# Kernel tuning notes

Measured on AMD Instinct MI355X. Metric: run time of the kernel, lower is better.

Reference implementation:

```python
import jax, jax.numpy as jnp
from jax import lax
import numpy as np

P = 0.25  # dropouto


def _lstm(x, Wih, Whh, b):
    """Standard torch-layout LSTM over [B, T, I]; gate order i,f,g,o.
    Wih: [4H, I], Whh: [4H, H], b: [4H] (= b_ih + b_hh). Returns [B, T, H]."""
    B, T, I = x.shape
    H = Whh.shape[1]
    # Precompute input contributions for all timesteps in one GEMM.
    xg = jnp.einsum('bti,gi->btg', x, Wih) + b  # [B, T, 4H]
    xg = jnp.swapaxes(xg, 0, 1)  # [T, B, 4H]

    def step(carry, xt):
        h, c = carry
        g = xt + h @ Whh.T  # [B, 4H]
        i, f, gg, o = jnp.split(g, 4, axis=-1)
        i = jax.nn.sigmoid(i)
        f = jax.nn.sigmoid(f)
        gg = jnp.tanh(gg)
        o = jax.nn.sigmoid(o)
        c = f * c + i * gg
        h = o * jnp.tanh(c)
        return (h, c), h

    h0 = jnp.zeros((B, H), x.dtype)
    c0 = jnp.zeros((B, H), x.dtype)
    _, hs = lax.scan(step, (h0, c0), xg)  # hs: [T, B, H]
    return jnp.swapaxes(hs, 0, 1)


def setup_inputs() -> dict:
    key = jax.random.key(0)
    ks = jax.random.split(key, 10)
    B, T = 512, 4096
    H1, H2 = 16, 1
    s = 0.25  # small init scale
    x = jax.random.normal(ks[0], (B, T, 1), jnp.float32)
    Wih1 = jax.random.normal(ks[1], (4 * H1, 1), jnp.float32) * s
    Whh1 = jax.random.normal(ks[2], (4 * H1, H1), jnp.float32) * s
    b1 = jax.random.normal(ks[3], (4 * H1,), jnp.float32) * s
    Wih2 = jax.random.normal(ks[4], (4 * H2, H1), jnp.float32) * s
    Whh2 = jax.random.normal(ks[5], (4 * H2, H2), jnp.float32) * s
    b2 = jax.random.normal(ks[6], (4 * H2,), jnp.float32) * s
    keep = 1.0 - P
    # Variational dropout masks: one mask per sequence, shared over time.
    mask1 = jax.random.bernoulli(ks[7], keep, (B, 1, H1)).astype(jnp.float32) / keep
    mask2 = jax.random.bernoulli(ks[8], keep, (B, 1, H2)).astype(jnp.float32) / keep
    return {"x": x, "Wih1": Wih1, "Whh1": Whh1, "b1": b1,
            "Wih2": Wih2, "Whh2": Whh2, "b2": b2,
            "mask1": mask1, "mask2": mask2}


def reference(x, Wih1, Whh1, b1, Wih2, Whh2, b2, mask1, mask2):
    out = _lstm(x, Wih1, Whh1, b1) * mask1   # dropouto on lstm1 output
    out = _lstm(out, Wih2, Whh2, b2) * mask2  # dropouto on lstm2 output
    return out  # [B, T, 1]
```

## Files before the change

### kernel.cpp

```cpp
#include <hip/hip_runtime.h>

typedef __fp16 f16x2 __attribute__((ext_vector_type(2)));

static __device__ __forceinline__ float rdlane(float v, int l) {
  return __uint_as_float(__builtin_amdgcn_readlane(__float_as_uint(v), (unsigned)l));
}
static __device__ __forceinline__ unsigned rdlane_u(unsigned v, int l) {
  return __builtin_amdgcn_readlane(v, (unsigned)l);
}

template <int CTRL>
static __device__ __forceinline__ float qperm(float v) {
  return __uint_as_float(__builtin_amdgcn_update_dpp(
      0u, __float_as_uint(v), CTRL, 0xF, 0xF, true));
}

static __device__ __forceinline__ float xswapadd32(float v) {
  float a = v, b;
  asm("v_mov_b32 %0, %1\n\t"
      "s_nop 1\n\t"
      "v_permlane32_swap_b32 %1, %0"
      : "=&v"(b), "+v"(a));
  return a + b;
}

static __device__ __forceinline__ float exp2a(float x) {
  float r;
  asm("v_exp_f32 %0, %1" : "=v"(r) : "v"(x));
  return r;
}
static __device__ __forceinline__ float rcpa(float x) {
  return __builtin_amdgcn_rcpf(x);
}

static __device__ __forceinline__ float dot2f(f16x2 a, unsigned bu, float c) {
#if __has_builtin(__builtin_amdgcn_fdot2)
  return __builtin_amdgcn_fdot2(a, __builtin_bit_cast(f16x2, bu), c, false);
#else
  float r = c;
  f16x2 b = __builtin_bit_cast(f16x2, bu);
  asm("v_dot2_f32_f16 %0, %1, %2, %0" : "+v"(r) : "v"(a), "v"(b));
  return r;
#endif
}

#define QP_XOR1 0xB1
#define QP_XOR2 0x4E
#define QP_XOR3 0x1B
#define QP_BC0  0x00
#define QP_BC1  0x55
#define QP_BC2  0xAA
#define QP_BC3  0xFF

__global__ __launch_bounds__(64, 1) void vdd_lstm_kernel(
    const float* __restrict__ x,
    const float* __restrict__ Wih1,
    const float* __restrict__ Whh1,
    const float* __restrict__ b1,
    const float* __restrict__ Wih2,
    const float* __restrict__ Whh2,
    const float* __restrict__ b2,
    const float* __restrict__ mask1,
    const float* __restrict__ mask2,
    float* __restrict__ out,
    int T) {
  const int b = blockIdx.x;
  const int lane = threadIdx.x;
  const int j = lane >> 2;
  const int gt = lane & 3;
  const int row = gt * 16 + j;

  const float LOG2E = 1.4426950408889634f;
  const bool isg = (gt == 2);
  const float sc = isg ? (-2.f * LOG2E) : (-LOG2E);
  const float aA = isg ? (-4.f * LOG2E) : 1.f;
  const float aC = isg ? (2.f * LOG2E) : 0.f;
  const bool isl1 = (lane == 1);

  f16x2 wh1[8];
#pragma unroll
  for (int m = 0; m < 8; ++m) {
    wh1[m].x = (__fp16)(Whh1[row * 16 + m] * sc);
    wh1[m].y = (__fp16)(Whh1[row * 16 + m + 8] * sc);
  }
  f16x2 wh2[8];
#pragma unroll
  for (int m = 0; m < 8; ++m) {
    wh2[m].x = (__fp16)(Wih2[gt * 16 + m] * mask1[b * 16 + m] * sc);
    wh2[m].y = (__fp16)(Wih2[gt * 16 + m + 8] * mask1[b * 16 + m + 8] * sc);
  }
  const float wih1 = Wih1[row] * sc;
  const float bb1  = b1[row] * sc;
  const float whh2 = Whh2[gt] * sc;
  const float bb2  = b2[gt] * sc;
  const float m2   = mask2[b];

  const float* xb = x + (size_t)b * T;
  float* ob = out + (size_t)b * T;

  float h = 0.f, cs = 0.f;
  float cs2 = 0.f, h2b = 0.f;

  const int NCH = T >> 6;
  const int tmax = T - 1;

  int idx0 = 1 + lane; idx0 = idx0 > tmax ? tmax : idx0;
  float xr = xb[idx0];

  {
    float x0 = xb[0];
    float pre = __fmaf_rn(wih1, x0, bb1);
    float a1 = __fmaf_rn(aA, rcpa(1.f + exp2a(pre)), aC);
    float g1 = qperm<QP_XOR2>(a1);
    float o1 = qperm<QP_XOR3>(a1);
    cs = a1 * g1;
    float th = __fmaf_rn(2.f, rcpa(1.f + exp2a(cs)), -1.f);
    h = o1 * th;
  }

  for (int ch = 0; ch < NCH; ++ch) {
    int idxn = (ch + 1) * 64 + 1 + lane;
    idxn = idxn > tmax ? tmax : idxn;
    float xnext = xb[idxn];

    float och = 0.f;

#pragma unroll 8
    for (int s = 0; s < 64; ++s) {
      float hsum = xswapadd32(h);
      float partner = hsum - h;
      f16x2 tp = __builtin_bit_cast(
          f16x2, __builtin_amdgcn_cvt_pkrtz(h, partner));
      unsigned tpu = __builtin_bit_cast(unsigned, tp);
      unsigned sp[8];
#pragma unroll
      for (int m = 0; m < 8; ++m) sp[m] = rdlane_u(tpu, 4 * m);

      float sx = rdlane(xr, s);

      float accA = __fmaf_rn(wih1, sx, bb1);
      float accB = dot2f(wh1[1], sp[1], 0.f);
      accA = dot2f(wh1[0], sp[0], accA);
      accB = dot2f(wh1[3], sp[3], accB);
      accA = dot2f(wh1[2], sp[2], accA);
      accB = dot2f(wh1[5], sp[5], accB);
      accA = dot2f(wh1[4], sp[4], accA);
      accB = dot2f(wh1[7], sp[7], accB);
      accA = dot2f(wh1[6], sp[6], accA);
      float pre = accA + accB;

      float accC = __fmaf_rn(whh2, h2b, bb2);
      float accD = dot2f(wh2[1], sp[1], 0.f);
      accC = dot2f(wh2[0], sp[0], accC);
      accD = dot2f(wh2[3], sp[3], accD);
      accC = dot2f(wh2[2], sp[2], accC);
      accD = dot2f(wh2[5], sp[5], accD);
      accC = dot2f(wh2[4], sp[4], accC);
      accD = dot2f(wh2[7], sp[7], accD);
      accC = dot2f(wh2[6], sp[6], accC);
      float pre2 = accC + accD;

      float a1 = __fmaf_rn(aA, rcpa(1.f + exp2a(pre)), aC);
      float f1 = qperm<QP_XOR1>(a1);
      float g1 = qperm<QP_XOR2>(a1);
      float o1 = qperm<QP_XOR3>(a1);
      cs = __fmaf_rn(f1, cs, a1 * g1);

      float a2 = __fmaf_rn(aA, rcpa(1.f + exp2a(pre2)), aC);
      float i2 = qperm<QP_BC0>(a2);
      float f2 = qperm<QP_BC1>(a2);
      float g2 = qperm<QP_BC2>(a2);
      float o2 = qperm<QP_BC3>(a2);
      cs2 = __fmaf_rn(f2, cs2, i2 * g2);

      float z = isl1 ? cs2 : cs;
      float thv = __fmaf_rn(2.f, rcpa(1.f + exp2a(z)), -1.f);
      float th2 = rdlane(thv, 1);
      float hn = o1 * thv;
      h2b = o2 * th2;
      float ov = h2b * m2;

      och = (lane == s) ? ov : och;
      h = hn;
    }

    ob[(ch << 6) + lane] = och;
    xr = xnext;
  }
}

extern "C" void kernel_launch(void* const* d_in, const int* in_sizes, int n_in,
                              void* d_out, int out_size, void* d_ws, size_t ws_size,
                              hipStream_t stream) {
  const float* x     = (const float*)d_in[0];
  const float* Wih1  = (const float*)d_in[1];
  const float* Whh1  = (const float*)d_in[2];
  const float* b1    = (const float*)d_in[3];
  const float* Wih2  = (const float*)d_in[4];
  const float* Whh2  = (const float*)d_in[5];
  const float* b2    = (const float*)d_in[6];
  const float* mask1 = (const float*)d_in[7];
  const float* mask2 = (const float*)d_in[8];
  float* out = (float*)d_out;

  const int B = in_sizes[8];
  const int T = in_sizes[0] / B;

  vdd_lstm_kernel<<<dim3(B), dim3(64), 0, stream>>>(
      x, Wih1, Whh1, b1, Wih2, Whh2, b2, mask1, mask2, out, T);
}
```

Baseline: 620.5 us.

## Skew LSTM2 one step behind LSTM1 to share a single tanh

Restructures the recurrence so layer 2 runs one timestep behind layer 1. Layer 2's pre-activation now takes the tanh of its cell state computed in the same lane-selected exp/rcp as layer 1's cell tanh, and its input dot products reuse the broadcast h vector. This moves layer 2's recurrent dependency off the serial critical path of each step. It adds a prologue step and shifted x indexing, and the output write alignment across chunk boundaries must stay correct.

```diff
diff --git a/kernel.cpp b/kernel.cpp
--- a/kernel.cpp
+++ b/kernel.cpp
@@ -98,18 +98,16 @@
   const float* xb = x + (size_t)b * T;
   float* ob = out + (size_t)b * T;
 
-  float h = 0.f, cs = 0.f;
-  float cs2 = 0.f, h2b = 0.f;
+  float h, cs;
+  float cs2p = 0.f;
+  float o2p = 0.f;
+  float och = 0.f;
 
   const int NCH = T >> 6;
   const int tmax = T - 1;
 
-  int idx0 = 1 + lane; idx0 = idx0 > tmax ? tmax : idx0;
-  float xr = xb[idx0];
-
   {
-    float x0 = xb[0];
-    float pre = __fmaf_rn(wih1, x0, bb1);
+    float pre = __fmaf_rn(wih1, xb[0], bb1);
     float a1 = __fmaf_rn(aA, rcpa(1.f + exp2a(pre)), aC);
     float g1 = qperm<QP_XOR2>(a1);
     float o1 = qperm<QP_XOR3>(a1);
@@ -118,74 +116,82 @@
     h = o1 * th;
   }
 
+  auto body = [&](float sx, bool doSel, int slot) {
+    float hsum = xswapadd32(h);
+    float partner = hsum - h;
+    f16x2 tp = __builtin_bit_cast(
+        f16x2, __builtin_amdgcn_cvt_pkrtz(h, partner));
+    unsigned tpu = __builtin_bit_cast(unsigned, tp);
+    unsigned sp[8];
+#pragma unroll
+    for (int m = 0; m < 8; ++m) sp[m] = rdlane_u(tpu, 4 * m);
+
+    float accA = __fmaf_rn(wih1, sx, bb1);
+    float accB = dot2f(wh1[1], sp[1], 0.f);
+    accA = dot2f(wh1[0], sp[0], accA);
+    accB = dot2f(wh1[3], sp[3], accB);
+    accA = dot2f(wh1[2], sp[2], accA);
+    accB = dot2f(wh1[5], sp[5], accB);
+    accA = dot2f(wh1[4], sp[4], accA);
+    accB = dot2f(wh1[7], sp[7], accB);
+    accA = dot2f(wh1[6], sp[6], accA);
+    float pre = accA + accB;
+
+    float accC = dot2f(wh2[0], sp[0], bb2);
+    float accD = dot2f(wh2[1], sp[1], 0.f);
+    accC = dot2f(wh2[2], sp[2], accC);
+    accD = dot2f(wh2[3], sp[3], accD);
+    accC = dot2f(wh2[4], sp[4], accC);
+    accD = dot2f(wh2[5], sp[5], accD);
+    accC = dot2f(wh2[6], sp[6], accC);
+    accD = dot2f(wh2[7], sp[7], accD);
+    float d2 = accC + accD;
+
+    float a1 = __fmaf_rn(aA, rcpa(1.f + exp2a(pre)), aC);
+    float f1 = qperm<QP_XOR1>(a1);
+    float g1 = qperm<QP_XOR2>(a1);
+    float o1 = qperm<QP_XOR3>(a1);
+    cs = __fmaf_rn(f1, cs, a1 * g1);
+
+    float z = isl1 ? cs2p : cs;
+    float thv = __fmaf_rn(2.f, rcpa(1.f + exp2a(z)), -1.f);
+    float hn = o1 * thv;
+    float th2 = rdlane(thv, 1);
+    float h2b = o2p * th2;
+
+    float pre2 = __fmaf_rn(whh2, h2b, d2);
+    float a2 = __fmaf_rn(aA, rcpa(1.f + exp2a(pre2)), aC);
+    float i2 = qperm<QP_BC0>(a2);
+    float f2 = qperm<QP_BC1>(a2);
+    float g2 = qperm<QP_BC2>(a2);
+    float o2n = qperm<QP_BC3>(a2);
+    cs2p = __fmaf_rn(f2, cs2p, i2 * g2);
+    o2p = o2n;
+
+    float ov = h2b * m2;
+    if (doSel) och = (lane == slot) ? ov : och;
+    h = hn;
+  };
+
+  int idx0 = 2 + lane;
+  idx0 = idx0 > tmax ? tmax : idx0;
+  float w = xb[idx0];
+
+  body(xb[1], false, 0);
+
   for (int ch = 0; ch < NCH; ++ch) {
-    int idxn = (ch + 1) * 64 + 1 + lane;
+    int idxn = (ch + 1) * 64 + 2 + lane;
     idxn = idxn > tmax ? tmax : idxn;
-    float xnext = xb[idxn];
-
-    float och = 0.f;
+    float wn = xb[idxn];
 
 #pragma unroll 8
-    for (int s = 0; s < 64; ++s) {
-      float hsum = xswapadd32(h);
-      float partner = hsum - h;
-      f16x2 tp = __builtin_bit_cast(
-          f16x2, __builtin_amdgcn_cvt_pkrtz(h, partner));
-      unsigned tpu = __builtin_bit_cast(unsigned, tp);
-      unsigned sp[8];
-#pragma unroll
-      for (int m = 0; m < 8; ++m) sp[m] = rdlane_u(tpu, 4 * m);
-
-      float sx = rdlane(xr, s);
-
-      float accA = __fmaf_rn(wih1, sx, bb1);
-      float accB = dot2f(wh1[1], sp[1], 0.f);
-      accA = dot2f(wh1[0], sp[0], accA);
-      accB = dot2f(wh1[3], sp[3], accB);
-      accA = dot2f(wh1[2], sp[2], accA);
-      accB = dot2f(wh1[5], sp[5], accB);
-      accA = dot2f(wh1[4], sp[4], accA);
-      accB = dot2f(wh1[7], sp[7], accB);
-      accA = dot2f(wh1[6], sp[6], accA);
-      float pre = accA + accB;
-
-      float accC = __fmaf_rn(whh2, h2b, bb2);
-      float accD = dot2f(wh2[1], sp[1], 0.f);
-      accC = dot2f(wh2[0], sp[0], accC);
-      accD = dot2f(wh2[3], sp[3], accD);
-      accC = dot2f(wh2[2], sp[2], accC);
-      accD = dot2f(wh2[5], sp[5], accD);
-      accC = dot2f(wh2[4], sp[4], accC);
-      accD = dot2f(wh2[7], sp[7], accD);
-      accC = dot2f(wh2[6], sp[6], accC);
-      float pre2 = accC + accD;
-
-      float a1 = __fmaf_rn(aA, rcpa(1.f + exp2a(pre)), aC);
-      float f1 = qperm<QP_XOR1>(a1);
-      float g1 = qperm<QP_XOR2>(a1);
-      float o1 = qperm<QP_XOR3>(a1);
-      cs = __fmaf_rn(f1, cs, a1 * g1);
-
-      float a2 = __fmaf_rn(aA, rcpa(1.f + exp2a(pre2)), aC);
-      float i2 = qperm<QP_BC0>(a2);
-      float f2 = qperm<QP_BC1>(a2);
-      float g2 = qperm<QP_BC2>(a2);
-      float o2 = qperm<QP_BC3>(a2);
-      cs2 = __fmaf_rn(f2, cs2, i2 * g2);
-
-      float z = isl1 ? cs2 : cs;
-      float thv = __fmaf_rn(2.f, rcpa(1.f + exp2a(z)), -1.f);
-      float th2 = rdlane(thv, 1);
-      float hn = o1 * thv;
-      h2b = o2 * th2;
-      float ov = h2b * m2;
-
-      och = (lane == s) ? ov : och;
-      h = hn;
+    for (int s2 = 0; s2 < 64; ++s2) {
+      float sx = rdlane(w, s2);
+      body(sx, true, s2);
     }
 
     ob[(ch << 6) + lane] = och;
-    xr = xnext;
+    w = wn;
   }
 }
 
```

New measurement: 576.5 us. -7.1%, faster.
